# Kernel optimization log

Measured on AMD Instinct MI355X. Metric: run time of the kernel, lower is better.

The kernel has to match this reference:

```python
import jax, jax.numpy as jnp
import numpy as np

LAMBDA = 0.7
RATIO = 3
EPS = 1e-6


def setup_inputs() -> dict:
    key = jax.random.key(0)
    k1, k2, k3 = jax.random.split(key, 3)
    bs, n, w, h = 8, 7, 640, 640
    preds = jax.random.normal(k1, (bs, n, w, h), dtype=jnp.float32)
    labels = jax.random.randint(k2, (bs, n, w, h), 0, 2, dtype=jnp.int32)
    training_mask = jax.random.randint(k3, (bs, w, h), 0, 2, dtype=jnp.int32)
    return {"preds": preds, "labels": labels, "training_mask": training_mask}


def _dice(S, G):
    # S, G: [C, P]; per-channel dice coefficient, then mean over channels
    num = 2.0 * jnp.sum(S * G, axis=-1)
    den = jnp.sum(S * S, axis=-1) + jnp.sum(G * G, axis=-1) + EPS
    return jnp.mean(num / den)


def _single_sample(pred, label, mask):
    # pred, label: [n, P]; mask: [P]
    P = pred.shape[-1]
    p = jax.nn.sigmoid(pred)
    pred_n = p[-1] * mask            # masked full-text prediction
    label_n = label[-1] * mask

    # --- OHEM mask M (cal_M): keep all positives + top (ratio*n_pos) hardest negatives ---
    pos = pred_n >= 0.5
    n_pos = jnp.sum(pos)
    n_neg_all = jnp.sum(~pos)
    k = n_pos * RATIO
    # sigmoid outputs are in (0,1); sentinel -1 pushes positives to the end of the descending sort
    neg_vals = jnp.where(pos, -1.0, pred_n)
    sorted_desc = -jnp.sort(-neg_vals)
    thr = sorted_desc[jnp.clip(k - 1, 0, P - 1)]  # k-th largest negative score
    ohem_active = (n_neg_all > k) & (k > 0)
    M = jnp.where(ohem_active, (pred_n >= thr).astype(jnp.float32), 1.0)

    # L_c: dice loss on OHEM-selected full-text map
    L_c = 1.0 - _dice((pred_n * M)[None, :], (label_n * M)[None, :])

    # L_s: dice loss on shrunk kernels, gated by predicted text region W
    W = (pred_n >= 0.5).astype(jnp.float32)
    L_s = 1.0 - _dice(p[:-1] * W, label[:-1] * W)

    loss = LAMBDA * L_c + (1.0 - LAMBDA) * L_s
    return L_c, L_s, loss


def reference(preds, labels, training_mask):
    bs, n, w, h = preds.shape
    preds = preds.reshape(bs, n, w * h)
    labels = labels.reshape(bs, n, w * h).astype(jnp.float32)
    mask = training_mask.reshape(bs, w * h).astype(jnp.float32)
    L_c, L_s, loss = jax.vmap(_single_sample)(preds, labels, mask)
    # reduction='mean'
    return L_c.mean(), L_s.mean(), loss.mean()
```

## Files before the change

kernel.cpp:

```cpp
#include <hip/hip_runtime.h>

#define BS   8
#define NCH  7
#define PX   409600
#define NBIN 65536
#define NCHK 256
#define WIN_LO 0x3000u
#define WIN_SZ 4096
#define EPSF 1e-6f

__device__ __forceinline__ float sigf(float x) {
    return 1.0f / (1.0f + __expf(-x));
}

__device__ __forceinline__ unsigned wred_u(unsigned v) {
    #pragma unroll
    for (int o = 32; o; o >>= 1) v += __shfl_down(v, o);
    return v;
}

__device__ __forceinline__ float wred_f(float v) {
    #pragma unroll
    for (int o = 32; o; o >>= 1) v += __shfl_down(v, o);
    return v;
}

__global__ __launch_bounds__(256) void k_main(const float* __restrict__ preds,
                                              const int* __restrict__ labels,
                                              const int* __restrict__ mask,
                                              unsigned* __restrict__ hist1,
                                              unsigned* __restrict__ chunks1,
                                              unsigned* __restrict__ n_pos,
                                              float* __restrict__ sums) {
    int b = blockIdx.y;
    const float* pr = preds + (size_t)b * NCH * PX;
    const int*   lb = labels + (size_t)b * NCH * PX;
    const int*   mk = mask + (size_t)b * PX;

    __shared__ unsigned lh[WIN_SZ];
    for (int j = threadIdx.x; j < WIN_SZ; j += 256) lh[j] = 0u;
    __syncthreads();

    unsigned pos_cnt = 0, zero_cnt = 0;
    float acc[18];
    #pragma unroll
    for (int j = 0; j < 18; j++) acc[j] = 0.f;

    for (int g = blockIdx.x * 256 + threadIdx.x; g < PX / 4; g += gridDim.x * 256) {
        int px = g * 4;
        float4 p6 = *(const float4*)(pr + 6 * PX + px);
        int4   m4 = *(const int4*)(mk + px);
        float mm[4]  = {(float)m4.x, (float)m4.y, (float)m4.z, (float)m4.w};
        float p6a[4] = {p6.x, p6.y, p6.z, p6.w};
        float W[4];
        #pragma unroll
        for (int u = 0; u < 4; u++) {
            float pn = sigf(p6a[u]) * mm[u];
            if (pn >= 0.5f) {
                pos_cnt++; W[u] = 1.0f;
            } else {
                W[u] = 0.0f;
                unsigned bits = __float_as_uint(pn);
                if (bits == 0u) {
                    zero_cnt++;
                } else {
                    unsigned hb = bits >> 16;
                    if (hb - WIN_LO < WIN_SZ) {
                        atomicAdd(&lh[hb - WIN_LO], 1u);
                    } else {
                        atomicAdd(&hist1[(size_t)b * NBIN + hb], 1u);
                        atomicAdd(&chunks1[b * NCHK + (hb >> 8)], 1u);
                    }
                }
            }
        }
        #pragma unroll
        for (int c = 0; c < 6; c++) {
            float4 pc4 = *(const float4*)(pr + c * PX + px);
            int4   lc4 = *(const int4*)(lb + c * PX + px);
            float pcs[4] = {pc4.x, pc4.y, pc4.z, pc4.w};
            float lcs[4] = {(float)lc4.x, (float)lc4.y, (float)lc4.z, (float)lc4.w};
            #pragma unroll
            for (int u = 0; u < 4; u++) {
                float s = sigf(pcs[u]);
                float l = lcs[u];
                acc[c]      += s * l * W[u];
                acc[6 + c]  += s * s * W[u];
                acc[12 + c] += l * W[u];
            }
        }
    }
    __syncthreads();

    for (int j = threadIdx.x; j < WIN_SZ; j += 256) {
        unsigned c = lh[j];
        if (c) atomicAdd(&hist1[(size_t)b * NBIN + WIN_LO + j], c);
    }
    __shared__ unsigned csum[256];
    {
        unsigned s = 0;
        int chunk = threadIdx.x >> 4, part = threadIdx.x & 15;
        const unsigned* base = &lh[chunk * 256 + part * 16];
        #pragma unroll
        for (int j = 0; j < 16; j++) s += base[j];
        csum[threadIdx.x] = s;
    }
    __syncthreads();
    if (threadIdx.x < 16) {
        unsigned s = 0;
        #pragma unroll
        for (int j = 0; j < 16; j++) s += csum[threadIdx.x * 16 + j];
        if (s) atomicAdd(&chunks1[b * NCHK + 48 + threadIdx.x], s);
    }

    __shared__ unsigned ws2[2][4];
    unsigned pv = wred_u(pos_cnt), zv = wred_u(zero_cnt);
    int lane = threadIdx.x & 63, wid = threadIdx.x >> 6;
    if (lane == 0) { ws2[0][wid] = pv; ws2[1][wid] = zv; }
    __syncthreads();
    if (threadIdx.x == 0) {
        unsigned pt = 0, zt = 0;
        #pragma unroll
        for (int w = 0; w < 4; w++) { pt += ws2[0][w]; zt += ws2[1][w]; }
        if (pt) atomicAdd(&n_pos[b], pt);
        if (zt) {
            atomicAdd(&hist1[(size_t)b * NBIN], zt);
            atomicAdd(&chunks1[b * NCHK], zt);
        }
    }

    __shared__ float red[4][18];
    #pragma unroll
    for (int j = 0; j < 18; j++) {
        float v = wred_f(acc[j]);
        if (lane == 0) red[wid][j] = v;
    }
    __syncthreads();
    if (threadIdx.x < 18) {
        float tot = red[0][threadIdx.x] + red[1][threadIdx.x] +
                    red[2][threadIdx.x] + red[3][threadIdx.x];
        atomicAdd(&sums[b * 21 + 3 + threadIdx.x], tot);
    }
}

__device__ void select2(const unsigned* __restrict__ chunks,
                        const unsigned* __restrict__ bins,
                        unsigned k, unsigned* out_bin, unsigned* out_rank) {
    __shared__ unsigned cs[256];
    __shared__ unsigned sel_c, sel_r;
    int t = threadIdx.x;
    cs[t] = chunks[t];
    __syncthreads();
    #pragma unroll
    for (int off = 1; off < 256; off <<= 1) {
        unsigned v = cs[t];
        unsigned a = (t + off < 256) ? cs[t + off] : 0u;
        __syncthreads();
        cs[t] = v + a;
        __syncthreads();
    }
    {
        unsigned sfx  = cs[t];
        unsigned sfx1 = (t < 255) ? cs[t + 1] : 0u;
        if (sfx >= k && sfx1 < k) { sel_c = (unsigned)t; sel_r = k - sfx1; }
    }
    __syncthreads();
    unsigned chunk = sel_c, krem = sel_r;
    cs[t] = bins[chunk * 256 + t];
    __syncthreads();
    #pragma unroll
    for (int off = 1; off < 256; off <<= 1) {
        unsigned v = cs[t];
        unsigned a = (t + off < 256) ? cs[t + off] : 0u;
        __syncthreads();
        cs[t] = v + a;
        __syncthreads();
    }
    {
        unsigned sfx  = cs[t];
        unsigned sfx1 = (t < 255) ? cs[t + 1] : 0u;
        if (sfx >= krem && sfx1 < krem) {
            *out_bin  = chunk * 256 + (unsigned)t;
            *out_rank = krem - sfx1;
        }
    }
    __syncthreads();
}

__global__ __launch_bounds__(256) void k_find_hi(const unsigned* __restrict__ hist1,
                                                 const unsigned* __restrict__ chunks1,
                                                 const unsigned* __restrict__ n_pos,
                                                 unsigned* __restrict__ hi_bin,
                                                 unsigned* __restrict__ rankv,
                                                 unsigned* __restrict__ activev,
                                                 float* __restrict__ thr) {
    int b = blockIdx.x;
    unsigned np_ = n_pos[b];
    unsigned k = np_ * 3u;
    unsigned nneg = (unsigned)PX - np_;
    if (!(nneg > k && k > 0u)) {
        if (threadIdx.x == 0) { activev[b] = 0u; thr[b] = -1.0f; }
        return;
    }
    __shared__ unsigned rb, rr;
    select2(chunks1 + b * NCHK, hist1 + (size_t)b * NBIN, k, &rb, &rr);
    if (threadIdx.x == 0) {
        activev[b] = 1u;
        hi_bin[b] = rb;
        rankv[b] = rr;
        if (rb == 0u) thr[b] = 0.0f;
    }
}

__global__ __launch_bounds__(256) void k_refine(const float* __restrict__ preds,
                                                const int* __restrict__ mask,
                                                const unsigned* __restrict__ hi_bin,
                                                const unsigned* __restrict__ activev,
                                                unsigned* __restrict__ hist2,
                                                unsigned* __restrict__ chunks2) {
    int b = blockIdx.y;
    if (!activev[b]) return;
    unsigned hi = hi_bin[b];
    if (hi == 0u) return;
    const float* pr = preds + ((size_t)b * NCH + 6) * PX;
    const int* mk = mask + (size_t)b * PX;
    unsigned* h2 = hist2 + (size_t)b * NBIN;
    unsigned* c2 = chunks2 + b * NCHK;
    for (int g = blockIdx.x * 256 + threadIdx.x; g < PX / 4; g += gridDim.x * 256) {
        int px = g * 4;
        float4 p6 = *(const float4*)(pr + px);
        int4   m4 = *(const int4*)(mk + px);
        float p6a[4] = {p6.x, p6.y, p6.z, p6.w};
        float mm[4]  = {(float)m4.x, (float)m4.y, (float)m4.z, (float)m4.w};
        #pragma unroll
        for (int u = 0; u < 4; u++) {
            float pn = sigf(p6a[u]) * mm[u];
            if (pn < 0.5f) {
                unsigned bits = __float_as_uint(pn);
                if ((bits >> 16) == hi) {
                    unsigned lo = bits & 0xFFFFu;
                    atomicAdd(&h2[lo], 1u);
                    atomicAdd(&c2[lo >> 8], 1u);
                }
            }
        }
    }
}

__global__ __launch_bounds__(256) void k_find_lo(const unsigned* __restrict__ hist2,
                                                 const unsigned* __restrict__ chunks2,
                                                 const unsigned* __restrict__ hi_bin,
                                                 const unsigned* __restrict__ rankv,
                                                 const unsigned* __restrict__ activev,
                                                 float* __restrict__ thr) {
    int b = blockIdx.x;
    if (!activev[b]) return;
    unsigned hi = hi_bin[b];
    if (hi == 0u) return;
    __shared__ unsigned rb, rr;
    select2(chunks2 + b * NCHK, hist2 + (size_t)b * NBIN, rankv[b], &rb, &rr);
    if (threadIdx.x == 0) thr[b] = __uint_as_float((hi << 16) | rb);
}

__global__ __launch_bounds__(256) void k_lc(const float* __restrict__ preds,
                                            const int* __restrict__ labels,
                                            const int* __restrict__ mask,
                                            const float* __restrict__ thr,
                                            float* __restrict__ sums) {
    int b = blockIdx.y;
    const float* pr = preds + ((size_t)b * NCH + 6) * PX;
    const int*   lb = labels + ((size_t)b * NCH + 6) * PX;
    const int*   mk = mask + (size_t)b * PX;
    float thr_b = thr[b];

    float a0 = 0.f, a1 = 0.f, a2 = 0.f;
    for (int g = blockIdx.x * 256 + threadIdx.x; g < PX / 4; g += gridDim.x * 256) {
        int px = g * 4;
        float4 p6 = *(const float4*)(pr + px);
        int4   l4 = *(const int4*)(lb + px);
        int4   m4 = *(const int4*)(mk + px);
        float p6a[4] = {p6.x, p6.y, p6.z, p6.w};
        float la[4]  = {(float)l4.x, (float)l4.y, (float)l4.z, (float)l4.w};
        float mm[4]  = {(float)m4.x, (float)m4.y, (float)m4.z, (float)m4.w};
        #pragma unroll
        for (int u = 0; u < 4; u++) {
            float pn = sigf(p6a[u]) * mm[u];
            float Mi = (pn >= thr_b) ? 1.0f : 0.0f;
            float ln = la[u] * mm[u];
            a0 += pn * ln * Mi;
            a1 += pn * pn * Mi;
            a2 += ln * Mi;
        }
    }
    __shared__ float red[4][3];
    int lane = threadIdx.x & 63, wid = threadIdx.x >> 6;
    float v0 = wred_f(a0), v1 = wred_f(a1), v2 = wred_f(a2);
    if (lane == 0) { red[wid][0] = v0; red[wid][1] = v1; red[wid][2] = v2; }
    __syncthreads();
    if (threadIdx.x < 3) {
        float tot = red[0][threadIdx.x] + red[1][threadIdx.x] +
                    red[2][threadIdx.x] + red[3][threadIdx.x];
        atomicAdd(&sums[b * 21 + threadIdx.x], tot);
    }
}

__global__ void k_final(const float* __restrict__ sums, float* __restrict__ out) {
    int t = threadIdx.x;
    float Lc = 0.f, Ls = 0.f;
    if (t < BS) {
        const float* s = sums + t * 21;
        Lc = 1.0f - (2.0f * s[0]) / (s[1] + s[2] + EPSF);
        float acc = 0.f;
        #pragma unroll
        for (int c = 0; c < 6; c++)
            acc += (2.0f * s[3 + c]) / (s[9 + c] + s[15 + c] + EPSF);
        Ls = 1.0f - acc * (1.0f / 6.0f);
    }
    #pragma unroll
    for (int o = 4; o; o >>= 1) { Lc += __shfl_down(Lc, o); Ls += __shfl_down(Ls, o); }
    if (t == 0) {
        float lc_m = Lc * (1.0f / (float)BS);
        float ls_m = Ls * (1.0f / (float)BS);
        out[0] = lc_m;
        out[1] = ls_m;
        out[2] = 0.7f * lc_m + 0.3f * ls_m;
    }
}

extern "C" void kernel_launch(void* const* d_in, const int* in_sizes, int n_in,
                              void* d_out, int out_size, void* d_ws, size_t ws_size,
                              hipStream_t stream) {
    const float* preds = (const float*)d_in[0];
    const int* labels  = (const int*)d_in[1];
    const int* mask    = (const int*)d_in[2];
    float* out = (float*)d_out;

    unsigned* hist1   = (unsigned*)d_ws;
    unsigned* hist2   = hist1 + (size_t)BS * NBIN;
    unsigned* chunks1 = hist2 + (size_t)BS * NBIN;
    unsigned* chunks2 = chunks1 + (size_t)BS * NCHK;
    unsigned* n_pos   = chunks2 + (size_t)BS * NCHK;
    unsigned* hi_bin  = n_pos + BS;
    unsigned* rankv   = hi_bin + BS;
    unsigned* activev = rankv + BS;
    float*    thr     = (float*)(activev + BS);
    float*    sums    = thr + BS;

    size_t zero_words = (size_t)2 * BS * NBIN + (size_t)2 * BS * NCHK + 5 * BS + (size_t)BS * 21;
    hipMemsetAsync(d_ws, 0, zero_words * sizeof(unsigned), stream);

    hipLaunchKernelGGL(k_main, dim3(100, BS), dim3(256), 0, stream,
                       preds, labels, mask, hist1, chunks1, n_pos, sums);

    hipLaunchKernelGGL(k_find_hi, dim3(BS), dim3(256), 0, stream,
                       hist1, chunks1, n_pos, hi_bin, rankv, activev, thr);

    hipLaunchKernelGGL(k_refine, dim3(32, BS), dim3(256), 0, stream,
                       preds, mask, hi_bin, activev, hist2, chunks2);

    hipLaunchKernelGGL(k_find_lo, dim3(BS), dim3(256), 0, stream,
                       hist2, chunks2, hi_bin, rankv, activev, thr);

    hipLaunchKernelGGL(k_lc, dim3(100, BS), dim3(256), 0, stream,
                       preds, labels, mask, thr, sums);

    hipLaunchKernelGGL(k_final, dim3(1), dim3(64), 0, stream, sums, out);
}
```

Baseline: 232.2 us.

## Fuse all OHEM dice loss stages into one cooperative kernel with grid syncs

Replaces the memset and six separate kernel launches with a single cooperative kernel. It zeroes the workspace in-kernel and separates the histogram, select, refine, select, Lc and final phases with grid-wide syncs. The grid is sized from occupancy, up to 2048 blocks. The main pass now issues all six channel loads up front for more memory-level parallelism. This removes launch gaps and the memset, at the cost of grid.sync overhead, register pressure under launch bounds (256,4), and idle blocks during the single-block select phases.

```diff
diff --git a/kernel.cpp b/kernel.cpp
--- a/kernel.cpp
+++ b/kernel.cpp
@@ -1,4 +1,7 @@
 #include <hip/hip_runtime.h>
+#include <hip/hip_cooperative_groups.h>
+
+namespace cg = cooperative_groups;
 
 #define BS   8
 #define NCH  7
@@ -8,6 +11,7 @@
 #define WIN_LO 0x3000u
 #define WIN_SZ 4096
 #define EPSF 1e-6f
+#define NT   256
 
 __device__ __forceinline__ float sigf(float x) {
     return 1.0f / (1.0f + __expf(-x));
@@ -23,124 +27,6 @@
     #pragma unroll
     for (int o = 32; o; o >>= 1) v += __shfl_down(v, o);
     return v;
-}
-
-__global__ __launch_bounds__(256) void k_main(const float* __restrict__ preds,
-                                              const int* __restrict__ labels,
-                                              const int* __restrict__ mask,
-                                              unsigned* __restrict__ hist1,
-                                              unsigned* __restrict__ chunks1,
-                                              unsigned* __restrict__ n_pos,
-                                              float* __restrict__ sums) {
-    int b = blockIdx.y;
-    const float* pr = preds + (size_t)b * NCH * PX;
-    const int*   lb = labels + (size_t)b * NCH * PX;
-    const int*   mk = mask + (size_t)b * PX;
-
-    __shared__ unsigned lh[WIN_SZ];
-    for (int j = threadIdx.x; j < WIN_SZ; j += 256) lh[j] = 0u;
-    __syncthreads();
-
-    unsigned pos_cnt = 0, zero_cnt = 0;
-    float acc[18];
-    #pragma unroll
-    for (int j = 0; j < 18; j++) acc[j] = 0.f;
-
-    for (int g = blockIdx.x * 256 + threadIdx.x; g < PX / 4; g += gridDim.x * 256) {
-        int px = g * 4;
-        float4 p6 = *(const float4*)(pr + 6 * PX + px);
-        int4   m4 = *(const int4*)(mk + px);
-        float mm[4]  = {(float)m4.x, (float)m4.y, (float)m4.z, (float)m4.w};
-        float p6a[4] = {p6.x, p6.y, p6.z, p6.w};
-        float W[4];
-        #pragma unroll
-        for (int u = 0; u < 4; u++) {
-            float pn = sigf(p6a[u]) * mm[u];
-            if (pn >= 0.5f) {
-                pos_cnt++; W[u] = 1.0f;
-            } else {
-                W[u] = 0.0f;
-                unsigned bits = __float_as_uint(pn);
-                if (bits == 0u) {
-                    zero_cnt++;
-                } else {
-                    unsigned hb = bits >> 16;
-                    if (hb - WIN_LO < WIN_SZ) {
-                        atomicAdd(&lh[hb - WIN_LO], 1u);
-                    } else {
-                        atomicAdd(&hist1[(size_t)b * NBIN + hb], 1u);
-                        atomicAdd(&chunks1[b * NCHK + (hb >> 8)], 1u);
-                    }
-                }
-            }
-        }
-        #pragma unroll
-        for (int c = 0; c < 6; c++) {
-            float4 pc4 = *(const float4*)(pr + c * PX + px);
-            int4   lc4 = *(const int4*)(lb + c * PX + px);
-            float pcs[4] = {pc4.x, pc4.y, pc4.z, pc4.w};
-            float lcs[4] = {(float)lc4.x, (float)lc4.y, (float)lc4.z, (float)lc4.w};
-            #pragma unroll
-            for (int u = 0; u < 4; u++) {
-                float s = sigf(pcs[u]);
-                float l = lcs[u];
-                acc[c]      += s * l * W[u];
-                acc[6 + c]  += s * s * W[u];
-                acc[12 + c] += l * W[u];
-            }
-        }
-    }
-    __syncthreads();
-
-    for (int j = threadIdx.x; j < WIN_SZ; j += 256) {
-        unsigned c = lh[j];
-        if (c) atomicAdd(&hist1[(size_t)b * NBIN + WIN_LO + j], c);
-    }
-    __shared__ unsigned csum[256];
-    {
-        unsigned s = 0;
-        int chunk = threadIdx.x >> 4, part = threadIdx.x & 15;
-        const unsigned* base = &lh[chunk * 256 + part * 16];
-        #pragma unroll
-        for (int j = 0; j < 16; j++) s += base[j];
-        csum[threadIdx.x] = s;
-    }
-    __syncthreads();
-    if (threadIdx.x < 16) {
-        unsigned s = 0;
-        #pragma unroll
-        for (int j = 0; j < 16; j++) s += csum[threadIdx.x * 16 + j];
-        if (s) atomicAdd(&chunks1[b * NCHK + 48 + threadIdx.x], s);
-    }
-
-    __shared__ unsigned ws2[2][4];
-    unsigned pv = wred_u(pos_cnt), zv = wred_u(zero_cnt);
-    int lane = threadIdx.x & 63, wid = threadIdx.x >> 6;
-    if (lane == 0) { ws2[0][wid] = pv; ws2[1][wid] = zv; }
-    __syncthreads();
-    if (threadIdx.x == 0) {
-        unsigned pt = 0, zt = 0;
-        #pragma unroll
-        for (int w = 0; w < 4; w++) { pt += ws2[0][w]; zt += ws2[1][w]; }
-        if (pt) atomicAdd(&n_pos[b], pt);
-        if (zt) {
-            atomicAdd(&hist1[(size_t)b * NBIN], zt);
-            atomicAdd(&chunks1[b * NCHK], zt);
-        }
-    }
-
-    __shared__ float red[4][18];
-    #pragma unroll
-    for (int j = 0; j < 18; j++) {
-        float v = wred_f(acc[j]);
-        if (lane == 0) red[wid][j] = v;
-    }
-    __syncthreads();
-    if (threadIdx.x < 18) {
-        float tot = red[0][threadIdx.x] + red[1][threadIdx.x] +
-                    red[2][threadIdx.x] + red[3][threadIdx.x];
-        atomicAdd(&sums[b * 21 + 3 + threadIdx.x], tot);
-    }
 }
 
 __device__ void select2(const unsigned* __restrict__ chunks,
@@ -187,143 +73,268 @@
     __syncthreads();
 }
 
-__global__ __launch_bounds__(256) void k_find_hi(const unsigned* __restrict__ hist1,
-                                                 const unsigned* __restrict__ chunks1,
-                                                 const unsigned* __restrict__ n_pos,
-                                                 unsigned* __restrict__ hi_bin,
-                                                 unsigned* __restrict__ rankv,
-                                                 unsigned* __restrict__ activev,
-                                                 float* __restrict__ thr) {
-    int b = blockIdx.x;
-    unsigned np_ = n_pos[b];
-    unsigned k = np_ * 3u;
-    unsigned nneg = (unsigned)PX - np_;
-    if (!(nneg > k && k > 0u)) {
-        if (threadIdx.x == 0) { activev[b] = 0u; thr[b] = -1.0f; }
-        return;
-    }
-    __shared__ unsigned rb, rr;
-    select2(chunks1 + b * NCHK, hist1 + (size_t)b * NBIN, k, &rb, &rr);
-    if (threadIdx.x == 0) {
-        activev[b] = 1u;
-        hi_bin[b] = rb;
-        rankv[b] = rr;
-        if (rb == 0u) thr[b] = 0.0f;
-    }
-}
-
-__global__ __launch_bounds__(256) void k_refine(const float* __restrict__ preds,
-                                                const int* __restrict__ mask,
-                                                const unsigned* __restrict__ hi_bin,
-                                                const unsigned* __restrict__ activev,
-                                                unsigned* __restrict__ hist2,
-                                                unsigned* __restrict__ chunks2) {
-    int b = blockIdx.y;
-    if (!activev[b]) return;
-    unsigned hi = hi_bin[b];
-    if (hi == 0u) return;
-    const float* pr = preds + ((size_t)b * NCH + 6) * PX;
-    const int* mk = mask + (size_t)b * PX;
-    unsigned* h2 = hist2 + (size_t)b * NBIN;
-    unsigned* c2 = chunks2 + b * NCHK;
-    for (int g = blockIdx.x * 256 + threadIdx.x; g < PX / 4; g += gridDim.x * 256) {
-        int px = g * 4;
-        float4 p6 = *(const float4*)(pr + px);
-        int4   m4 = *(const int4*)(mk + px);
-        float p6a[4] = {p6.x, p6.y, p6.z, p6.w};
-        float mm[4]  = {(float)m4.x, (float)m4.y, (float)m4.z, (float)m4.w};
+__global__ __launch_bounds__(256, 4) void k_fused(
+        const float* __restrict__ preds, const int* __restrict__ labels,
+        const int* __restrict__ mask,
+        unsigned* __restrict__ hist1, unsigned* __restrict__ hist2,
+        unsigned* __restrict__ chunks1, unsigned* __restrict__ chunks2,
+        unsigned* __restrict__ n_pos, unsigned* __restrict__ hi_bin,
+        unsigned* __restrict__ rankv, unsigned* __restrict__ activev,
+        float* __restrict__ thr, float* __restrict__ sums,
+        float* __restrict__ out) {
+    cg::grid_group grid = cg::this_grid();
+    const int tid = threadIdx.x;
+    const unsigned nblk = gridDim.x;
+    const unsigned nthr = nblk * NT;
+    const unsigned gtid = blockIdx.x * NT + tid;
+    const unsigned bpb  = nblk >> 3;
+
+    __shared__ unsigned lh[WIN_SZ];
+    __shared__ unsigned csum[256];
+    __shared__ unsigned ws2[2][4];
+    __shared__ float    red[4][18];
+
+    {
+        const size_t zw = (size_t)2 * BS * NBIN + (size_t)2 * BS * NCHK
+                        + 5 * BS + (size_t)BS * 21;
+        for (size_t i = gtid; i < zw; i += nthr) hist1[i] = 0u;
+    }
+    for (int j = tid; j < WIN_SZ; j += NT) lh[j] = 0u;
+    grid.sync();
+
+    {
+        const unsigned b  = blockIdx.x / bpb;
+        const unsigned cb = blockIdx.x % bpb;
+        const float* pr = preds + (size_t)b * NCH * PX;
+        const int*   lb = labels + (size_t)b * NCH * PX;
+        const int*   mk = mask + (size_t)b * PX;
+
+        unsigned pos_cnt = 0, zero_cnt = 0;
+        float acc[18];
         #pragma unroll
-        for (int u = 0; u < 4; u++) {
-            float pn = sigf(p6a[u]) * mm[u];
-            if (pn < 0.5f) {
-                unsigned bits = __float_as_uint(pn);
-                if ((bits >> 16) == hi) {
-                    unsigned lo = bits & 0xFFFFu;
-                    atomicAdd(&h2[lo], 1u);
-                    atomicAdd(&c2[lo >> 8], 1u);
+        for (int j = 0; j < 18; j++) acc[j] = 0.f;
+
+        for (unsigned g = cb * NT + tid; g < PX / 4; g += bpb * NT) {
+            int px = (int)g * 4;
+            float4 p6 = *(const float4*)(pr + 6 * PX + px);
+            int4   m4 = *(const int4*)(mk + px);
+            float4 pc[6];
+            int4   lc[6];
+            #pragma unroll
+            for (int c = 0; c < 6; c++) pc[c] = *(const float4*)(pr + c * PX + px);
+            #pragma unroll
+            for (int c = 0; c < 6; c++) lc[c] = *(const int4*)(lb + c * PX + px);
+
+            float mm[4]  = {(float)m4.x, (float)m4.y, (float)m4.z, (float)m4.w};
+            float p6a[4] = {p6.x, p6.y, p6.z, p6.w};
+            float W[4];
+            #pragma unroll
+            for (int u = 0; u < 4; u++) {
+                float pn = sigf(p6a[u]) * mm[u];
+                if (pn >= 0.5f) {
+                    pos_cnt++; W[u] = 1.0f;
+                } else {
+                    W[u] = 0.0f;
+                    unsigned bits = __float_as_uint(pn);
+                    if (bits == 0u) {
+                        zero_cnt++;
+                    } else {
+                        unsigned hb = bits >> 16;
+                        if (hb - WIN_LO < WIN_SZ) {
+                            atomicAdd(&lh[hb - WIN_LO], 1u);
+                        } else {
+                            atomicAdd(&hist1[(size_t)b * NBIN + hb], 1u);
+                            atomicAdd(&chunks1[b * NCHK + (hb >> 8)], 1u);
+                        }
+                    }
                 }
             }
-        }
-    }
-}
-
-__global__ __launch_bounds__(256) void k_find_lo(const unsigned* __restrict__ hist2,
-                                                 const unsigned* __restrict__ chunks2,
-                                                 const unsigned* __restrict__ hi_bin,
-                                                 const unsigned* __restrict__ rankv,
-                                                 const unsigned* __restrict__ activev,
-                                                 float* __restrict__ thr) {
-    int b = blockIdx.x;
-    if (!activev[b]) return;
-    unsigned hi = hi_bin[b];
-    if (hi == 0u) return;
-    __shared__ unsigned rb, rr;
-    select2(chunks2 + b * NCHK, hist2 + (size_t)b * NBIN, rankv[b], &rb, &rr);
-    if (threadIdx.x == 0) thr[b] = __uint_as_float((hi << 16) | rb);
-}
-
-__global__ __launch_bounds__(256) void k_lc(const float* __restrict__ preds,
-                                            const int* __restrict__ labels,
-                                            const int* __restrict__ mask,
-                                            const float* __restrict__ thr,
-                                            float* __restrict__ sums) {
-    int b = blockIdx.y;
-    const float* pr = preds + ((size_t)b * NCH + 6) * PX;
-    const int*   lb = labels + ((size_t)b * NCH + 6) * PX;
-    const int*   mk = mask + (size_t)b * PX;
-    float thr_b = thr[b];
-
-    float a0 = 0.f, a1 = 0.f, a2 = 0.f;
-    for (int g = blockIdx.x * 256 + threadIdx.x; g < PX / 4; g += gridDim.x * 256) {
-        int px = g * 4;
-        float4 p6 = *(const float4*)(pr + px);
-        int4   l4 = *(const int4*)(lb + px);
-        int4   m4 = *(const int4*)(mk + px);
-        float p6a[4] = {p6.x, p6.y, p6.z, p6.w};
-        float la[4]  = {(float)l4.x, (float)l4.y, (float)l4.z, (float)l4.w};
-        float mm[4]  = {(float)m4.x, (float)m4.y, (float)m4.z, (float)m4.w};
+
+            #pragma unroll
+            for (int c = 0; c < 6; c++) {
+                float pcs[4] = {pc[c].x, pc[c].y, pc[c].z, pc[c].w};
+                float lcs[4] = {(float)lc[c].x, (float)lc[c].y,
+                                (float)lc[c].z, (float)lc[c].w};
+                #pragma unroll
+                for (int u = 0; u < 4; u++) {
+                    float s = sigf(pcs[u]);
+                    float l = lcs[u];
+                    acc[c]      += s * l * W[u];
+                    acc[6 + c]  += s * s * W[u];
+                    acc[12 + c] += l * W[u];
+                }
+            }
+        }
+        __syncthreads();
+
+        for (int j = tid; j < WIN_SZ; j += NT) {
+            unsigned c = lh[j];
+            if (c) atomicAdd(&hist1[(size_t)b * NBIN + WIN_LO + j], c);
+        }
+        {
+            unsigned s = 0;
+            int chunk = tid >> 4, part = tid & 15;
+            const unsigned* base = &lh[chunk * 256 + part * 16];
+            #pragma unroll
+            for (int j = 0; j < 16; j++) s += base[j];
+            csum[tid] = s;
+        }
+        __syncthreads();
+        if (tid < 16) {
+            unsigned s = 0;
+            #pragma unroll
+            for (int j = 0; j < 16; j++) s += csum[tid * 16 + j];
+            if (s) atomicAdd(&chunks1[b * NCHK + 48 + tid], s);
+        }
+
+        unsigned pv = wred_u(pos_cnt), zv = wred_u(zero_cnt);
+        int lane = tid & 63, wid = tid >> 6;
+        if (lane == 0) { ws2[0][wid] = pv; ws2[1][wid] = zv; }
+        __syncthreads();
+        if (tid == 0) {
+            unsigned pt = 0, zt = 0;
+            #pragma unroll
+            for (int w = 0; w < 4; w++) { pt += ws2[0][w]; zt += ws2[1][w]; }
+            if (pt) atomicAdd(&n_pos[b], pt);
+            if (zt) {
+                atomicAdd(&hist1[(size_t)b * NBIN], zt);
+                atomicAdd(&chunks1[b * NCHK], zt);
+            }
+        }
+
         #pragma unroll
-        for (int u = 0; u < 4; u++) {
-            float pn = sigf(p6a[u]) * mm[u];
-            float Mi = (pn >= thr_b) ? 1.0f : 0.0f;
-            float ln = la[u] * mm[u];
-            a0 += pn * ln * Mi;
-            a1 += pn * pn * Mi;
-            a2 += ln * Mi;
-        }
-    }
-    __shared__ float red[4][3];
-    int lane = threadIdx.x & 63, wid = threadIdx.x >> 6;
-    float v0 = wred_f(a0), v1 = wred_f(a1), v2 = wred_f(a2);
-    if (lane == 0) { red[wid][0] = v0; red[wid][1] = v1; red[wid][2] = v2; }
-    __syncthreads();
-    if (threadIdx.x < 3) {
-        float tot = red[0][threadIdx.x] + red[1][threadIdx.x] +
-                    red[2][threadIdx.x] + red[3][threadIdx.x];
-        atomicAdd(&sums[b * 21 + threadIdx.x], tot);
-    }
-}
-
-__global__ void k_final(const float* __restrict__ sums, float* __restrict__ out) {
-    int t = threadIdx.x;
-    float Lc = 0.f, Ls = 0.f;
-    if (t < BS) {
-        const float* s = sums + t * 21;
-        Lc = 1.0f - (2.0f * s[0]) / (s[1] + s[2] + EPSF);
-        float acc = 0.f;
+        for (int j = 0; j < 18; j++) {
+            float v = wred_f(acc[j]);
+            if (lane == 0) red[wid][j] = v;
+        }
+        __syncthreads();
+        if (tid < 18) {
+            float tot = red[0][tid] + red[1][tid] + red[2][tid] + red[3][tid];
+            atomicAdd(&sums[b * 21 + 3 + tid], tot);
+        }
+    }
+    grid.sync();
+
+    if (blockIdx.x < BS) {
+        int b = blockIdx.x;
+        unsigned np_ = n_pos[b];
+        unsigned k = np_ * 3u;
+        unsigned nneg = (unsigned)PX - np_;
+        if (!(nneg > k && k > 0u)) {
+            if (tid == 0) { activev[b] = 0u; thr[b] = -1.0f; }
+        } else {
+            __shared__ unsigned rb, rr;
+            select2(chunks1 + b * NCHK, hist1 + (size_t)b * NBIN, k, &rb, &rr);
+            if (tid == 0) {
+                activev[b] = 1u;
+                hi_bin[b] = rb;
+                rankv[b] = rr;
+                if (rb == 0u) thr[b] = 0.0f;
+            }
+        }
+    }
+    grid.sync();
+
+    for (int b3 = 0; b3 < BS; b3++) {
+        if (!activev[b3]) continue;
+        unsigned hi = hi_bin[b3];
+        if (hi == 0u) continue;
+        const float* pr = preds + ((size_t)b3 * NCH + 6) * PX;
+        const int*   mk = mask + (size_t)b3 * PX;
+        unsigned* h2 = hist2 + (size_t)b3 * NBIN;
+        unsigned* c2 = chunks2 + b3 * NCHK;
+        for (unsigned g = gtid; g < PX / 4; g += nthr) {
+            int px = (int)g * 4;
+            float4 p6 = *(const float4*)(pr + px);
+            int4   m4 = *(const int4*)(mk + px);
+            float p6a[4] = {p6.x, p6.y, p6.z, p6.w};
+            float mm[4]  = {(float)m4.x, (float)m4.y, (float)m4.z, (float)m4.w};
+            #pragma unroll
+            for (int u = 0; u < 4; u++) {
+                float pn = sigf(p6a[u]) * mm[u];
+                if (pn < 0.5f) {
+                    unsigned bits = __float_as_uint(pn);
+                    if ((bits >> 16) == hi) {
+                        unsigned lo = bits & 0xFFFFu;
+                        atomicAdd(&h2[lo], 1u);
+                        atomicAdd(&c2[lo >> 8], 1u);
+                    }
+                }
+            }
+        }
+    }
+    grid.sync();
+
+    if (blockIdx.x < BS) {
+        int b = blockIdx.x;
+        if (activev[b] && hi_bin[b] != 0u) {
+            __shared__ unsigned rb2, rr2;
+            select2(chunks2 + b * NCHK, hist2 + (size_t)b * NBIN, rankv[b], &rb2, &rr2);
+            if (tid == 0) thr[b] = __uint_as_float((hi_bin[b] << 16) | rb2);
+        }
+    }
+    grid.sync();
+
+    {
+        const unsigned b  = blockIdx.x / bpb;
+        const unsigned cb = blockIdx.x % bpb;
+        const float* pr = preds + ((size_t)b * NCH + 6) * PX;
+        const int*   lb = labels + ((size_t)b * NCH + 6) * PX;
+        const int*   mk = mask + (size_t)b * PX;
+        float thr_b = thr[b];
+
+        float a0 = 0.f, a1 = 0.f, a2 = 0.f;
+        for (unsigned g = cb * NT + tid; g < PX / 4; g += bpb * NT) {
+            int px = (int)g * 4;
+            float4 p6 = *(const float4*)(pr + px);
+            int4   l4 = *(const int4*)(lb + px);
+            int4   m4 = *(const int4*)(mk + px);
+            float p6a[4] = {p6.x, p6.y, p6.z, p6.w};
+            float la[4]  = {(float)l4.x, (float)l4.y, (float)l4.z, (float)l4.w};
+            float mm[4]  = {(float)m4.x, (float)m4.y, (float)m4.z, (float)m4.w};
+            #pragma unroll
+            for (int u = 0; u < 4; u++) {
+                float pn = sigf(p6a[u]) * mm[u];
+                float Mi = (pn >= thr_b) ? 1.0f : 0.0f;
+                float ln = la[u] * mm[u];
+                a0 += pn * ln * Mi;
+                a1 += pn * pn * Mi;
+                a2 += ln * Mi;
+            }
+        }
+        int lane = tid & 63, wid = tid >> 6;
+        float v0 = wred_f(a0), v1 = wred_f(a1), v2 = wred_f(a2);
+        __syncthreads();
+        if (lane == 0) { red[wid][0] = v0; red[wid][1] = v1; red[wid][2] = v2; }
+        __syncthreads();
+        if (tid < 3) {
+            float tot = red[0][tid] + red[1][tid] + red[2][tid] + red[3][tid];
+            atomicAdd(&sums[b * 21 + tid], tot);
+        }
+    }
+    grid.sync();
+
+    if (blockIdx.x == 0) {
+        int t = tid;
+        float Lc = 0.f, Ls = 0.f;
+        if (t < BS) {
+            const float* s = sums + t * 21;
+            Lc = 1.0f - (2.0f * s[0]) / (s[1] + s[2] + EPSF);
+            float a = 0.f;
+            #pragma unroll
+            for (int c = 0; c < 6; c++)
+                a += (2.0f * s[3 + c]) / (s[9 + c] + s[15 + c] + EPSF);
+            Ls = 1.0f - a * (1.0f / 6.0f);
+        }
         #pragma unroll
-        for (int c = 0; c < 6; c++)
-            acc += (2.0f * s[3 + c]) / (s[9 + c] + s[15 + c] + EPSF);
-        Ls = 1.0f - acc * (1.0f / 6.0f);
-    }
-    #pragma unroll
-    for (int o = 4; o; o >>= 1) { Lc += __shfl_down(Lc, o); Ls += __shfl_down(Ls, o); }
-    if (t == 0) {
-        float lc_m = Lc * (1.0f / (float)BS);
-        float ls_m = Ls * (1.0f / (float)BS);
-        out[0] = lc_m;
-        out[1] = ls_m;
-        out[2] = 0.7f * lc_m + 0.3f * ls_m;
+        for (int o = 4; o; o >>= 1) { Lc += __shfl_down(Lc, o); Ls += __shfl_down(Ls, o); }
+        if (t == 0) {
+            float lc_m = Lc * (1.0f / (float)BS);
+            float ls_m = Ls * (1.0f / (float)BS);
+            out[0] = lc_m;
+            out[1] = ls_m;
+            out[2] = 0.7f * lc_m + 0.3f * ls_m;
+        }
     }
 }
 
@@ -346,23 +357,19 @@
     float*    thr     = (float*)(activev + BS);
     float*    sums    = thr + BS;
 
-    size_t zero_words = (size_t)2 * BS * NBIN + (size_t)2 * BS * NCHK + 5 * BS + (size_t)BS * 21;
-    hipMemsetAsync(d_ws, 0, zero_words * sizeof(unsigned), stream);
-
-    hipLaunchKernelGGL(k_main, dim3(100, BS), dim3(256), 0, stream,
-                       preds, labels, mask, hist1, chunks1, n_pos, sums);
-
-    hipLaunchKernelGGL(k_find_hi, dim3(BS), dim3(256), 0, stream,
-                       hist1, chunks1, n_pos, hi_bin, rankv, activev, thr);
-
-    hipLaunchKernelGGL(k_refine, dim3(32, BS), dim3(256), 0, stream,
-                       preds, mask, hi_bin, activev, hist2, chunks2);
-
-    hipLaunchKernelGGL(k_find_lo, dim3(BS), dim3(256), 0, stream,
-                       hist2, chunks2, hi_bin, rankv, activev, thr);
-
-    hipLaunchKernelGGL(k_lc, dim3(100, BS), dim3(256), 0, stream,
-                       preds, labels, mask, thr, sums);
-
-    hipLaunchKernelGGL(k_final, dim3(1), dim3(64), 0, stream, sums, out);
-}
+    static int maxBlk = 0;
+    if (maxBlk == 0) {
+        hipError_t e = hipOccupancyMaxActiveBlocksPerMultiprocessor(&maxBlk, k_fused, NT, 0);
+        if (e != hipSuccess || maxBlk < 1) maxBlk = 1;
+    }
+    int nblk = maxBlk * 256;
+    if (nblk > 2048) nblk = 2048;
+    nblk &= ~7;
+    if (nblk < 8) nblk = 8;
+
+    void* args[] = { (void*)&preds, (void*)&labels, (void*)&mask,
+                     (void*)&hist1, (void*)&hist2, (void*)&chunks1, (void*)&chunks2,
+                     (void*)&n_pos, (void*)&hi_bin, (void*)&rankv, (void*)&activev,
+                     (void*)&thr, (void*)&sums, (void*)&out };
+    hipLaunchCooperativeKernel((void*)k_fused, dim3(nblk), dim3(NT), args, 0, stream);
+}
```

New measurement: 539.9 us. 2.32x slower.
